# Performance work log

Hardware: AMD Instinct MI355X
Metric: run time of the kernel (lower is better)

Reference implementation:

```python
import jax, jax.numpy as jnp
import numpy as np

THRESHOLD = 0.59275


def setup_inputs() -> dict:
    key = jax.random.key(0)
    k4, k8, k16 = jax.random.split(key, 3)
    # [n_color_distances=3, batch=64, num_patches, box, box]
    x4 = jax.random.uniform(k4, (3, 64, 4096, 4, 4), dtype=jnp.float32)
    x8 = jax.random.uniform(k8, (3, 64, 1024, 8, 8), dtype=jnp.float32)
    x16 = jax.random.uniform(k16, (3, 64, 256, 16, 16), dtype=jnp.float32)
    return {"x4": x4, "x8": x8, "x16": x16}


def _percolation_q(x):
    # x: [C, B, P, b, b] -> per-patch occupancy fraction -> threshold -> mean over patches
    b = x.shape[-1]
    frac = jnp.sum(x, axis=(-2, -1)) / float(b * b)          # [C, B, P]
    q = (frac >= THRESHOLD).astype(jnp.float32)               # [C, B, P]
    return jnp.mean(q, axis=-1)                               # [C, B]


def reference(x4, x8, x16):
    # Output mirrors list[color][box] of [batch] vectors: one [n_color, batch]
    # array per box size.
    return (_percolation_q(x4), _percolation_q(x8), _percolation_q(x16))
```

## Files before the change

### kernel.cpp

```cpp
#include <hip/hip_runtime.h>


#define PERC_THRESHOLD 0.59275f

template <int B>
__device__ __forceinline__ void perc_body(const float* __restrict__ x,
                                          float* __restrict__ out,
                                          float invP) {
    constexpr int LPP = (B * B) / 4;
    constexpr int ITERS = 8;
    const int tid = threadIdx.x;
    const int lane = tid & 63;
    const float4* __restrict__ xv = (const float4*)x;
    const long long base = (long long)blockIdx.x * (256 * ITERS);
    const float thr = PERC_THRESHOLD * (float)(B * B);

    int cnt = 0;
#pragma unroll
    for (int j = 0; j < ITERS; ++j) {
        float4 v = xv[base + (long long)j * 256 + tid];
        float s = (v.x + v.y) + (v.z + v.w);
#pragma unroll
        for (int off = 1; off < LPP; off <<= 1)
            s += __shfl_xor(s, off, 64);
        if ((lane & (LPP - 1)) == 0 && s >= thr) cnt++;
    }

#pragma unroll
    for (int off = 32; off > 0; off >>= 1)
        cnt += __shfl_down(cnt, off, 64);

    __shared__ int wsum[4];
    if (lane == 0) wsum[tid >> 6] = cnt;
    __syncthreads();
    if (tid == 0) {
        float total = (float)(wsum[0] + wsum[1] + wsum[2] + wsum[3]);
        atomicAdd(&out[blockIdx.x >> 3], total * invP);
    }
}

__global__ __launch_bounds__(256)
void PercolationQ_31885837205970_kernel(const float* __restrict__ x4,
                                        const float* __restrict__ x8,
                                        const float* __restrict__ x16,
                                        float* __restrict__ out) {
    if (blockIdx.y == 0)      perc_body<4>(x4,  out,        1.0f / 4096.0f);
    else if (blockIdx.y == 1) perc_body<8>(x8,  out + 192,  1.0f / 1024.0f);
    else                      perc_body<16>(x16, out + 384, 1.0f / 256.0f);
}

extern "C" void kernel_launch(void* const* d_in, const int* in_sizes, int n_in,
                              void* d_out, int out_size, void* d_ws, size_t ws_size,
                              hipStream_t stream) {
    const float* x4  = (const float*)d_in[0];
    const float* x8  = (const float*)d_in[1];
    const float* x16 = (const float*)d_in[2];
    float* out = (float*)d_out;

    hipMemsetAsync(d_out, 0, (size_t)out_size * sizeof(float), stream);

    dim3 grid(1536, 3), block(256);
    hipLaunchKernelGGL(PercolationQ_31885837205970_kernel, grid, block, 0, stream,
                       x4, x8, x16, out);
}
```

Measured before the change: 159.6 us.

## Process all three inputs per block with batched loads and ballot-popcount counting

Each block now handles slices of all three inputs. It issues six float4 loads per input back to back so more memory requests are in flight, and counts passing patches with a wavefront ballot and popcount instead of a shuffle reduction. The grid becomes 2048 one-dimensional blocks with launch bounds requesting occupancy 8, and each block makes 18 atomics instead of one. The aim is more memory-level parallelism and less reduction overhead, at the cost of more atomics and more register pressure.

```diff
diff --git a/kernel.cpp b/kernel.cpp
--- a/kernel.cpp
+++ b/kernel.cpp
@@ -4,49 +4,75 @@
 #define PERC_THRESHOLD 0.59275f
 
 template <int B>
-__device__ __forceinline__ void perc_body(const float* __restrict__ x,
-                                          float* __restrict__ out,
-                                          float invP) {
+__device__ __forceinline__ int patch_count(float4 v, int lane) {
     constexpr int LPP = (B * B) / 4;
-    constexpr int ITERS = 8;
-    const int tid = threadIdx.x;
-    const int lane = tid & 63;
-    const float4* __restrict__ xv = (const float4*)x;
-    const long long base = (long long)blockIdx.x * (256 * ITERS);
+    float s = (v.x + v.y) + (v.z + v.w);
+#pragma unroll
+    for (int off = 1; off < LPP; off <<= 1)
+        s += __shfl_xor(s, off, 64);
     const float thr = PERC_THRESHOLD * (float)(B * B);
-
-    int cnt = 0;
-#pragma unroll
-    for (int j = 0; j < ITERS; ++j) {
-        float4 v = xv[base + (long long)j * 256 + tid];
-        float s = (v.x + v.y) + (v.z + v.w);
-#pragma unroll
-        for (int off = 1; off < LPP; off <<= 1)
-            s += __shfl_xor(s, off, 64);
-        if ((lane & (LPP - 1)) == 0 && s >= thr) cnt++;
-    }
-
-#pragma unroll
-    for (int off = 32; off > 0; off >>= 1)
-        cnt += __shfl_down(cnt, off, 64);
-
-    __shared__ int wsum[4];
-    if (lane == 0) wsum[tid >> 6] = cnt;
-    __syncthreads();
-    if (tid == 0) {
-        float total = (float)(wsum[0] + wsum[1] + wsum[2] + wsum[3]);
-        atomicAdd(&out[blockIdx.x >> 3], total * invP);
-    }
+    unsigned long long m = __ballot((lane & (LPP - 1)) == 0 && s >= thr);
+    return (int)__popcll(m);
 }
 
-__global__ __launch_bounds__(256)
+__global__ __launch_bounds__(256, 8)
 void PercolationQ_31885837205970_kernel(const float* __restrict__ x4,
                                         const float* __restrict__ x8,
                                         const float* __restrict__ x16,
                                         float* __restrict__ out) {
-    if (blockIdx.y == 0)      perc_body<4>(x4,  out,        1.0f / 4096.0f);
-    else if (blockIdx.y == 1) perc_body<8>(x8,  out + 192,  1.0f / 1024.0f);
-    else                      perc_body<16>(x16, out + 384, 1.0f / 256.0f);
+    const int tid = threadIdx.x;
+    const int lane = tid & 63;
+    const int wid = tid >> 6;
+    const int b = blockIdx.x;
+
+    __shared__ int wsum[4][18];
+
+    const float4* __restrict__ p4 = (const float4*)x4;
+    const float4* __restrict__ p8 = (const float4*)x8;
+    const float4* __restrict__ p16 = (const float4*)x16;
+
+    float4 v[6];
+
+#pragma unroll
+    for (int j = 0; j < 6; ++j)
+        v[j] = p4[(long long)(b + j * 2048) * 256 + tid];
+#pragma unroll
+    for (int j = 0; j < 6; ++j) {
+        int c = patch_count<4>(v[j], lane);
+        if (lane == 0) wsum[wid][j] = c;
+    }
+
+#pragma unroll
+    for (int j = 0; j < 6; ++j)
+        v[j] = p8[(long long)(b + j * 2048) * 256 + tid];
+#pragma unroll
+    for (int j = 0; j < 6; ++j) {
+        int c = patch_count<8>(v[j], lane);
+        if (lane == 0) wsum[wid][6 + j] = c;
+    }
+
+#pragma unroll
+    for (int j = 0; j < 6; ++j)
+        v[j] = p16[(long long)(b + j * 2048) * 256 + tid];
+#pragma unroll
+    for (int j = 0; j < 6; ++j) {
+        int c = patch_count<16>(v[j], lane);
+        if (lane == 0) wsum[wid][12 + j] = c;
+    }
+
+    __syncthreads();
+
+    if (tid < 18) {
+        const int input = tid / 6;
+        const int j = tid - input * 6;
+        float total = (float)(wsum[0][tid] + wsum[1][tid] +
+                              wsum[2][tid] + wsum[3][tid]);
+        const float invP = (input == 0) ? (1.0f / 4096.0f)
+                         : (input == 1) ? (1.0f / 1024.0f)
+                                        : (1.0f / 256.0f);
+        const int row = (b >> 6) + j * 32;
+        atomicAdd(&out[input * 192 + row], total * invP);
+    }
 }
 
 extern "C" void kernel_launch(void* const* d_in, const int* in_sizes, int n_in,
@@ -59,7 +85,7 @@
 
     hipMemsetAsync(d_out, 0, (size_t)out_size * sizeof(float), stream);
 
-    dim3 grid(1536, 3), block(256);
+    dim3 grid(2048), block(256);
     hipLaunchKernelGGL(PercolationQ_31885837205970_kernel, grid, block, 0, stream,
                        x4, x8, x16, out);
 }
```

Measured after the change: 166.1 us. +4.1%, slower.

## Assign whole patches per thread instead of cross-lane shuffle reductions

Applied to the files above, without the earlier changes.

Replaces the coalesced float4-per-thread scheme with per-thread contiguous patch reads: each thread sums entire 4x4 or 8x8 patches, or half a 16x16 patch, so most wave shuffles disappear. The grid is flattened to 1920 one-dimensional blocks, with the 16x16 blocks scheduled first, and launch bounds request higher occupancy. The cost is strided per-thread float4 loads that coalesce poorly across a wavefront, which may hurt DRAM efficiency on this memory-bound kernel.

```diff
diff --git a/kernel.cpp b/kernel.cpp
--- a/kernel.cpp
+++ b/kernel.cpp
@@ -3,27 +3,62 @@
 
 #define PERC_THRESHOLD 0.59275f
 
-template <int B>
-__device__ __forceinline__ void perc_body(const float* __restrict__ x,
-                                          float* __restrict__ out,
-                                          float invP) {
-    constexpr int LPP = (B * B) / 4;
-    constexpr int ITERS = 8;
+__device__ __forceinline__ float f4sum(float4 v) {
+    return (v.x + v.y) + (v.z + v.w);
+}
+
+__device__ __forceinline__ float group4(const float4* __restrict__ p) {
+    float4 a = p[0], b = p[1], c = p[2], d = p[3];
+    return (f4sum(a) + f4sum(b)) + (f4sum(c) + f4sum(d));
+}
+
+__global__ __launch_bounds__(256, 8)
+void PercolationQ_31885837205970_kernel(const float* __restrict__ x4,
+                                        const float* __restrict__ x8,
+                                        const float* __restrict__ x16,
+                                        float* __restrict__ out) {
     const int tid = threadIdx.x;
     const int lane = tid & 63;
-    const float4* __restrict__ xv = (const float4*)x;
-    const long long base = (long long)blockIdx.x * (256 * ITERS);
-    const float thr = PERC_THRESHOLD * (float)(B * B);
+    const int b = blockIdx.x;
 
     int cnt = 0;
+    int outIdx;
+    float invP;
+
+    if (b < 384) {
+        const int g = b * 256 + tid;
+        const float4* __restrict__ p = (const float4*)x16 + (long long)g * 32;
+        float g0 = group4(p +  0), g1 = group4(p +  4);
+        float g2 = group4(p +  8), g3 = group4(p + 12);
+        float g4 = group4(p + 16), g5 = group4(p + 20);
+        float g6 = group4(p + 24), g7 = group4(p + 28);
+        float s = ((g0 + g1) + (g2 + g3)) + ((g4 + g5) + (g6 + g7));
+        s += __shfl_xor(s, 1, 64);
+        const float thr = PERC_THRESHOLD * 256.0f;
+        if ((tid & 1) == 0 && s >= thr) cnt = 1;
+        outIdx = 384 + (b >> 1);
+        invP = 1.0f / 256.0f;
+    } else if (b < 1152) {
+        const int bb = b - 384;
+        const int g = bb * 256 + tid;
+        const float4* __restrict__ p = (const float4*)x4 + (long long)g * 16;
+        const float thr = PERC_THRESHOLD * 16.0f;
 #pragma unroll
-    for (int j = 0; j < ITERS; ++j) {
-        float4 v = xv[base + (long long)j * 256 + tid];
-        float s = (v.x + v.y) + (v.z + v.w);
-#pragma unroll
-        for (int off = 1; off < LPP; off <<= 1)
-            s += __shfl_xor(s, off, 64);
-        if ((lane & (LPP - 1)) == 0 && s >= thr) cnt++;
+        for (int k = 0; k < 4; ++k) {
+            float s = group4(p + k * 4);
+            if (s >= thr) cnt++;
+        }
+        outIdx = bb >> 2;
+        invP = 1.0f / 4096.0f;
+    } else {
+        const int bb = b - 1152;
+        const int g = bb * 256 + tid;
+        const float4* __restrict__ p = (const float4*)x8 + (long long)g * 16;
+        float s = (group4(p) + group4(p + 4)) + (group4(p + 8) + group4(p + 12));
+        const float thr = PERC_THRESHOLD * 64.0f;
+        if (s >= thr) cnt = 1;
+        outIdx = 192 + (bb >> 2);
+        invP = 1.0f / 1024.0f;
     }
 
 #pragma unroll
@@ -35,18 +70,8 @@
     __syncthreads();
     if (tid == 0) {
         float total = (float)(wsum[0] + wsum[1] + wsum[2] + wsum[3]);
-        atomicAdd(&out[blockIdx.x >> 3], total * invP);
+        atomicAdd(&out[outIdx], total * invP);
     }
-}
-
-__global__ __launch_bounds__(256)
-void PercolationQ_31885837205970_kernel(const float* __restrict__ x4,
-                                        const float* __restrict__ x8,
-                                        const float* __restrict__ x16,
-                                        float* __restrict__ out) {
-    if (blockIdx.y == 0)      perc_body<4>(x4,  out,        1.0f / 4096.0f);
-    else if (blockIdx.y == 1) perc_body<8>(x8,  out + 192,  1.0f / 1024.0f);
-    else                      perc_body<16>(x16, out + 384, 1.0f / 256.0f);
 }
 
 extern "C" void kernel_launch(void* const* d_in, const int* in_sizes, int n_in,
@@ -59,7 +84,7 @@
 
     hipMemsetAsync(d_out, 0, (size_t)out_size * sizeof(float), stream);
 
-    dim3 grid(1536, 3), block(256);
+    dim3 grid(1920), block(256);
     hipLaunchKernelGGL(PercolationQ_31885837205970_kernel, grid, block, 0, stream,
                        x4, x8, x16, out);
 }
```

Result: slower. 171.7 us (+7.6%).

## Stream inputs through LDS with async global_load_lds double buffering per wave

Applied to the files above, without the earlier changes.

Replaces the per-block direct float4 loads and shuffle reductions with a persistent 256-block grid. Each wave streams 16KB chunks of all three tensors into swizzled, double-buffered LDS using global_load_lds, overlapping the next chunk's load with summing the current one. Per-patch sums are done in registers and thresholds are counted with ballot/popcount, which removes most cross-lane shuffles. The risk is lower occupancy from the large 128KB LDS footprint and fewer blocks to hide latency, plus hand-tuned vmcnt waits that must track the outstanding-load count exactly.

```diff
diff --git a/kernel.cpp b/kernel.cpp
--- a/kernel.cpp
+++ b/kernel.cpp
@@ -1,52 +1,104 @@
 #include <hip/hip_runtime.h>
+#include <stdint.h>
 
 
 #define PERC_THRESHOLD 0.59275f
 
-template <int B>
-__device__ __forceinline__ void perc_body(const float* __restrict__ x,
-                                          float* __restrict__ out,
-                                          float invP) {
-    constexpr int LPP = (B * B) / 4;
-    constexpr int ITERS = 8;
-    const int tid = threadIdx.x;
-    const int lane = tid & 63;
-    const float4* __restrict__ xv = (const float4*)x;
-    const long long base = (long long)blockIdx.x * (256 * ITERS);
-    const float thr = PERC_THRESHOLD * (float)(B * B);
+typedef const __attribute__((address_space(1))) uint32_t* gas_ptr;
+typedef __attribute__((address_space(3))) uint32_t* las_ptr;
 
-    int cnt = 0;
+template <int N>
+__device__ __forceinline__ void wait_vm() {
+    asm volatile("s_waitcnt vmcnt(%0)" ::"n"(N) : "memory");
+    __builtin_amdgcn_sched_barrier(0);
+}
+
+__device__ __forceinline__ float f4sum(float4 v) { return (v.x + v.y) + (v.z + v.w); }
+
+__device__ __forceinline__ void stage16(const float4* __restrict__ gbase,
+                                        float4* lbase, int q, int r) {
 #pragma unroll
-    for (int j = 0; j < ITERS; ++j) {
-        float4 v = xv[base + (long long)j * 256 + tid];
-        float s = (v.x + v.y) + (v.z + v.w);
-#pragma unroll
-        for (int off = 1; off < LPP; off <<= 1)
-            s += __shfl_xor(s, off, 64);
-        if ((lane & (LPP - 1)) == 0 && s >= thr) cnt++;
-    }
-
-#pragma unroll
-    for (int off = 32; off > 0; off >>= 1)
-        cnt += __shfl_down(cnt, off, 64);
-
-    __shared__ int wsum[4];
-    if (lane == 0) wsum[tid >> 6] = cnt;
-    __syncthreads();
-    if (tid == 0) {
-        float total = (float)(wsum[0] + wsum[1] + wsum[2] + wsum[3]);
-        atomicAdd(&out[blockIdx.x >> 3], total * invP);
+    for (int k = 0; k < 16; ++k) {
+        const int src = k * 64 + q * 16 + (r ^ ((4 * k + q) & 15));
+        __builtin_amdgcn_global_load_lds((gas_ptr)(gbase + src),
+                                         (las_ptr)(lbase + k * 64), 16, 0, 0);
     }
 }
+
+template <int TT>
+__device__ __forceinline__ int consume_phase(const float4* __restrict__ lbase, int lane) {
+    const int c = lane & 15;
+    const float4* lp = lbase + lane * 16;
+    float g[4];
+#pragma unroll
+    for (int k = 0; k < 4; ++k) {
+        float4 a = lp[(4 * k + 0) ^ c];
+        float4 b = lp[(4 * k + 1) ^ c];
+        float4 d = lp[(4 * k + 2) ^ c];
+        float4 e = lp[(4 * k + 3) ^ c];
+        g[k] = (f4sum(a) + f4sum(b)) + (f4sum(d) + f4sum(e));
+    }
+    if constexpr (TT == 0) {
+        const float thr = PERC_THRESHOLD * 16.0f;
+        int cnt = 0;
+#pragma unroll
+        for (int k = 0; k < 4; ++k)
+            cnt += (int)__popcll(__ballot(g[k] >= thr));
+        return cnt;
+    } else if constexpr (TT == 1) {
+        const float thr = PERC_THRESHOLD * 64.0f;
+        float s = (g[0] + g[1]) + (g[2] + g[3]);
+        return (int)__popcll(__ballot(s >= thr));
+    } else {
+        const float thr = PERC_THRESHOLD * 256.0f;
+        float s = (g[0] + g[1]) + (g[2] + g[3]);
+        s += __shfl_xor(s, 1, 64);
+        s += __shfl_xor(s, 2, 64);
+        return (int)__popcll(__ballot(((lane & 3) == 0) && (s >= thr)));
+    }
+}
+
+#define PH_T(ph) ((ph) / 3)
+#define PH_S(ph) ((ph) % 3)
+#define PH_INVP(ph) (PH_T(ph) == 0 ? (1.0f / 4096.0f) \
+                   : PH_T(ph) == 1 ? (1.0f / 1024.0f) : (1.0f / 256.0f))
+#define STAGE(ph) stage16(gin[PH_T(ph)] + (long long)(w + PH_S(ph) * 1024) * 1024, \
+                          (((ph) & 1) ? wbB : wbA), q, r)
+#define CONSUME(ph)                                                               \
+    do {                                                                          \
+        int cnt_ = consume_phase<PH_T(ph)>((((ph) & 1) ? wbB : wbA), lane);       \
+        if (lane == 0) {                                                          \
+            const int P_ = w + PH_S(ph) * 1024;  \
+            atomicAdd(&out[PH_T(ph) * 192 + (P_ >> 4)], (float)cnt_ * PH_INVP(ph)); \
+        }                                                                         \
+    } while (0)
 
 __global__ __launch_bounds__(256)
 void PercolationQ_31885837205970_kernel(const float* __restrict__ x4,
                                         const float* __restrict__ x8,
                                         const float* __restrict__ x16,
                                         float* __restrict__ out) {
-    if (blockIdx.y == 0)      perc_body<4>(x4,  out,        1.0f / 4096.0f);
-    else if (blockIdx.y == 1) perc_body<8>(x8,  out + 192,  1.0f / 1024.0f);
-    else                      perc_body<16>(x16, out + 384, 1.0f / 256.0f);
+    __shared__ float4 ldsA[4096];
+    __shared__ float4 ldsB[4096];
+    const int tid = threadIdx.x;
+    const int lane = tid & 63;
+    const int wid = tid >> 6;
+    const int w = blockIdx.x * 4 + wid;
+    const int q = lane >> 4, r = lane & 15;
+    float4* wbA = &ldsA[wid * 1024];
+    float4* wbB = &ldsB[wid * 1024];
+    const float4* gin[3] = {(const float4*)x4, (const float4*)x8, (const float4*)x16};
+
+    STAGE(0);
+    STAGE(1); wait_vm<16>(); CONSUME(0);
+    STAGE(2); wait_vm<17>(); CONSUME(1);
+    STAGE(3); wait_vm<17>(); CONSUME(2);
+    STAGE(4); wait_vm<17>(); CONSUME(3);
+    STAGE(5); wait_vm<17>(); CONSUME(4);
+    STAGE(6); wait_vm<17>(); CONSUME(5);
+    STAGE(7); wait_vm<17>(); CONSUME(6);
+    STAGE(8); wait_vm<17>(); CONSUME(7);
+              wait_vm<1>();  CONSUME(8);
 }
 
 extern "C" void kernel_launch(void* const* d_in, const int* in_sizes, int n_in,
@@ -59,7 +111,7 @@
 
     hipMemsetAsync(d_out, 0, (size_t)out_size * sizeof(float), stream);
 
-    dim3 grid(1536, 3), block(256);
+    dim3 grid(256), block(256);
     hipLaunchKernelGGL(PercolationQ_31885837205970_kernel, grid, block, 0, stream,
                        x4, x8, x16, out);
 }
```

After: 162.5 us. About the same (+1.8%).
